# Kernel tuning notes

Measured on AMD Instinct MI355X. Metric: run time of the kernel, lower is better.

## Reference

```python
import jax, jax.numpy as jnp
import numpy as np

# dims: B batch, C tokens-per-patch, S num_patches, T input_channel(=output_channel), D d_model, P pool_size
B, C, S, T, D, P = 8, 512, 64, 128, 256, 8
EPS = 1e-5


def _cos_attn(pooled, keys):
    # pooled: (B,S,F), keys: (P,F) -> softmax over pool of cosine similarities: (B,S,P)
    pn = pooled / (jnp.linalg.norm(pooled, axis=-1, keepdims=True) + 1e-8)
    kn = keys / (jnp.linalg.norm(keys, axis=-1, keepdims=True) + 1e-8)
    return jax.nn.softmax(jnp.einsum('bsf,pf->bsp', pn, kn), axis=-1)


def setup_inputs() -> dict:
    key = jax.random.key(0)
    ks = jax.random.split(key, 5)
    sc = lambda k, shape, fan: jax.random.normal(k, shape, jnp.float32) * np.float32(1.0 / np.sqrt(fan))
    return {
        'x': jax.random.normal(ks[0], (B, C, S, T), jnp.float32),
        'gamma': jnp.ones((T,), jnp.float32),
        'beta': jnp.zeros((T,), jnp.float32),
        'keys1': sc(ks[1], (P, T), T),      # routing keys, WeightPool1
        'Wp1': sc(ks[2], (P, D, T), T),     # weight bank, T -> D
        'bp1': jnp.zeros((P, D), jnp.float32),
        'keys2': sc(ks[3], (P, D), D),      # routing keys, WeightPool2
        'Wp2': sc(ks[4], (P, T, D), D),     # weight bank, D -> T
        'bp2': jnp.zeros((P, T), jnp.float32),
    }


def reference(x, gamma, beta, keys1, Wp1, bp1, keys2, Wp2, bp2):
    # x_proj = Identity(x) since input_channel == output_channel
    # BatchNorm2d over channel T (x permuted to (B,T,S,C)) == normalize x over dims (0,1,2)
    mean = x.mean(axis=(0, 1, 2))
    var = x.var(axis=(0, 1, 2))  # biased, as torch BN training stats
    y = (x - mean) * jax.lax.rsqrt(var + EPS) * gamma + beta  # (B,C,S,T)

    # WeightPool1: pool over C, cosine-route into weight bank
    a1 = _cos_attn(y.mean(axis=1), keys1)            # (B,S,P)
    w1 = jnp.einsum('bsp,pdt->bsdt', a1, Wp1)        # (B,S,D,T)
    b1 = jnp.einsum('bsp,pd->bsd', a1, bp1)          # (B,S,D)

    y = jnp.einsum('bcst,bsdt->bcsd', y, w1) + b1[:, None]  # (B,C,S,D)
    y = jax.nn.relu(y)
    # dropout: inference mode (identity)

    # WeightPool2
    a2 = _cos_attn(y.mean(axis=1), keys2)            # (B,S,P)
    w2 = jnp.einsum('bsp,ptd->bstd', a2, Wp2)        # (B,S,T,D)
    b2 = jnp.einsum('bsp,pt->bst', a2, bp2)          # (B,S,T)

    y = jnp.einsum('bcsd,bstd->bcst', y, w2) + b2[:, None]  # (B,C,S,T)
    return (x + y, w1, w2)
```

## Files before the change

kernel.cpp:

```cpp
#include <hip/hip_runtime.h>
#include <hip/hip_bf16.h>

#define BB 8
#define CC 512
#define SS 64
#define TT 128
#define DD 256
#define PP 8
#define BS (BB*SS)
#define NSTAT (BB*CC*SS)
#define EPSV 1e-5f

typedef float f32x4 __attribute__((ext_vector_type(4)));
typedef __bf16 bf16x8 __attribute__((ext_vector_type(8)));

__device__ __forceinline__ unsigned short f2bf(float f) {
  unsigned u = __float_as_uint(f);
  u += 0x7FFFu + ((u >> 16) & 1u);
  return (unsigned short)(u >> 16);
}
__device__ __forceinline__ float bf2f(unsigned short h) {
  return __uint_as_float(((unsigned)h) << 16);
}

__global__ __launch_bounds__(256) void k1_stats(const float* __restrict__ x,
    float* __restrict__ csum_part, float* __restrict__ ssq_part,
    unsigned short* __restrict__ xbf) {
  int bid = blockIdx.x;
  int bs = bid >> 2, cq = bid & 3;
  int b = bs >> 6, s = bs & 63;
  const float* xb = x + ((size_t)b * CC * SS + s) * TT;
  unsigned short* xo = xbf + ((size_t)b * CC * SS + s) * TT;
  int tid = threadIdx.x;
  int t4 = tid & 31, coff = tid >> 5;
  float cs0=0,cs1=0,cs2=0,cs3=0, ss0=0,ss1=0,ss2=0,ss3=0;
  #pragma unroll 8
  for (int k = 0; k < 16; k++) {
    int c = cq*128 + coff + k*8;
    float4 v = *reinterpret_cast<const float4*>(xb + (size_t)c*(SS*TT) + t4*4);
    ushort4 o; o.x=f2bf(v.x); o.y=f2bf(v.y); o.z=f2bf(v.z); o.w=f2bf(v.w);
    *reinterpret_cast<ushort4*>(xo + (size_t)c*(SS*TT) + t4*4) = o;
    cs0 += v.x; cs1 += v.y; cs2 += v.z; cs3 += v.w;
    ss0 += v.x*v.x; ss1 += v.y*v.y; ss2 += v.z*v.z; ss3 += v.w*v.w;
  }
  __shared__ float4 redC[256];
  __shared__ float4 redS[256];
  redC[tid] = make_float4(cs0,cs1,cs2,cs3);
  redS[tid] = make_float4(ss0,ss1,ss2,ss3);
  __syncthreads();
  if (tid < 32) {
    #pragma unroll
    for (int j = 1; j < 8; j++) {
      float4 a = redC[tid + j*32], bq = redS[tid + j*32];
      cs0+=a.x; cs1+=a.y; cs2+=a.z; cs3+=a.w;
      ss0+=bq.x; ss1+=bq.y; ss2+=bq.z; ss3+=bq.w;
    }
    int t0 = tid*4;
    csum_part[(size_t)(t0+0)*2048 + bid] = cs0;
    csum_part[(size_t)(t0+1)*2048 + bid] = cs1;
    csum_part[(size_t)(t0+2)*2048 + bid] = cs2;
    csum_part[(size_t)(t0+3)*2048 + bid] = cs3;
    ssq_part[(size_t)(t0+0)*2048 + bid] = ss0;
    ssq_part[(size_t)(t0+1)*2048 + bid] = ss1;
    ssq_part[(size_t)(t0+2)*2048 + bid] = ss2;
    ssq_part[(size_t)(t0+3)*2048 + bid] = ss3;
  }
}

__global__ __launch_bounds__(256) void k1b_reduce(
    const float* __restrict__ csum_part, const float* __restrict__ ssq_part,
    float* __restrict__ sumt, float* __restrict__ sumsq) {
  int t = blockIdx.x, tid = threadIdx.x;
  const float* cp = csum_part + (size_t)t*2048;
  const float* sp = ssq_part + (size_t)t*2048;
  float cs = 0.f, ss = 0.f;
  #pragma unroll
  for (int k=0;k<8;k++) { cs += cp[tid + k*256]; ss += sp[tid + k*256]; }
  #pragma unroll
  for (int off=32; off; off>>=1) { cs += __shfl_xor(cs,off); ss += __shfl_xor(ss,off); }
  __shared__ float redc[4], reds[4];
  int wave = tid >> 6, lane = tid & 63;
  if (lane == 0) { redc[wave] = cs; reds[wave] = ss; }
  __syncthreads();
  if (tid == 0) {
    sumt[t]  = redc[0]+redc[1]+redc[2]+redc[3];
    sumsq[t] = reds[0]+reds[1]+reds[2]+reds[3];
  }
}

__global__ __launch_bounds__(256) void k2_route1(
    const float* __restrict__ sumt, const float* __restrict__ sumsq,
    const float* __restrict__ csum_part, const float* __restrict__ gamma,
    const float* __restrict__ beta, const float* __restrict__ keys1,
    const float* __restrict__ Wp1, const float* __restrict__ bp1,
    float* __restrict__ w1out, unsigned short* __restrict__ w1bf,
    float* __restrict__ b1) {
  int bid = blockIdx.x;
  int bs = bid >> 2, q = bid & 3;
  int tid = threadIdx.x;
  __shared__ float a1s[PP];
  if (tid < 64) {
    float pv0, pv1;
    {
      int t = tid;
      float4 c4v = *reinterpret_cast<const float4*>(csum_part + (size_t)t*2048 + bs*4);
      float cs = c4v.x + c4v.y + c4v.z + c4v.w;
      float m = sumt[t] * (1.f/NSTAT);
      float var = sumsq[t]*(1.f/NSTAT) - m*m;
      float g = gamma[t] * rsqrtf(var + EPSV);
      pv0 = (cs*(1.f/CC) - m)*g + beta[t];
    }
    {
      int t = tid + 64;
      float4 c4v = *reinterpret_cast<const float4*>(csum_part + (size_t)t*2048 + bs*4);
      float cs = c4v.x + c4v.y + c4v.z + c4v.w;
      float m = sumt[t] * (1.f/NSTAT);
      float var = sumsq[t]*(1.f/NSTAT) - m*m;
      float g = gamma[t] * rsqrtf(var + EPSV);
      pv1 = (cs*(1.f/CC) - m)*g + beta[t];
    }
    float ssq = pv0*pv0 + pv1*pv1;
    #pragma unroll
    for (int off=32; off; off>>=1) ssq += __shfl_xor(ssq, off);
    float pn = sqrtf(ssq) + 1e-8f;
    float lg[PP];
    #pragma unroll
    for (int p=0;p<PP;p++) {
      float k0 = keys1[p*TT + tid], k1 = keys1[p*TT + tid + 64];
      float dot = pv0*k0 + pv1*k1;
      float kn = k0*k0 + k1*k1;
      #pragma unroll
      for (int off=32; off; off>>=1) { dot += __shfl_xor(dot,off); kn += __shfl_xor(kn,off); }
      lg[p] = dot / (pn * (sqrtf(kn) + 1e-8f));
    }
    if (tid == 0) {
      float mx = lg[0];
      #pragma unroll
      for (int p=1;p<PP;p++) mx = fmaxf(mx, lg[p]);
      float se = 0.f, e[PP];
      #pragma unroll
      for (int p=0;p<PP;p++){ e[p] = __expf(lg[p]-mx); se += e[p]; }
      float inv = 1.f/se;
      #pragma unroll
      for (int p=0;p<PP;p++) a1s[p] = e[p]*inv;
    }
  }
  __syncthreads();
  float a[PP];
  #pragma unroll
  for (int p=0;p<PP;p++) a[p]=a1s[p];
  #pragma unroll
  for (int i=0;i<8;i++) {
    int idx = tid + i*256;
    int dr = idx >> 5, c4 = idx & 31;
    size_t roff = (size_t)(q*64+dr)*TT + c4*4;
    size_t off = (size_t)bs*(DD*TT) + roff;
    float4 accv = make_float4(0.f,0.f,0.f,0.f);
    #pragma unroll
    for (int p=0;p<PP;p++) {
      float4 v = *reinterpret_cast<const float4*>(Wp1 + (size_t)p*(DD*TT) + roff);
      accv.x += a[p]*v.x; accv.y += a[p]*v.y; accv.z += a[p]*v.z; accv.w += a[p]*v.w;
    }
    *reinterpret_cast<float4*>(w1out + off) = accv;
    ushort4 o; o.x=f2bf(accv.x); o.y=f2bf(accv.y); o.z=f2bf(accv.z); o.w=f2bf(accv.w);
    *reinterpret_cast<ushort4*>(w1bf + off) = o;
  }
  if (tid < 64) {
    int d = q*64 + tid;
    float bacc = 0.f;
    #pragma unroll
    for (int p=0;p<PP;p++) bacc += a[p]*bp1[p*DD + d];
    b1[(size_t)bs*DD + d] = bacc;
  }
}

__global__ __launch_bounds__(512) void k3_gemm1(
    const unsigned short* __restrict__ xbf, const float* __restrict__ sumt,
    const float* __restrict__ sumsq, const float* __restrict__ gamma,
    const float* __restrict__ beta, const unsigned short* __restrict__ w1bf,
    const float* __restrict__ b1, unsigned short* __restrict__ zbf,
    float* __restrict__ p2part) {
  int bid = blockIdx.x;
  int bs = bid >> 2, mt = bid & 3;
  int b = bs >> 6, s = bs & 63;
  __shared__ unsigned short lA[128*128];
  __shared__ unsigned short lB[256*128];
  __shared__ float mean_s[TT], g_s[TT], beta_s[TT];
  int tid = threadIdx.x;
  if (tid < TT) {
    float m = sumt[tid]*(1.f/NSTAT);
    float var = sumsq[tid]*(1.f/NSTAT) - m*m;
    mean_s[tid] = m;
    g_s[tid] = gamma[tid]*rsqrtf(var+EPSV);
    beta_s[tid] = beta[tid];
  }
  __syncthreads();
  char* lAc = reinterpret_cast<char*>(lA);
  char* lBc = reinterpret_cast<char*>(lB);
  auto bn2 = [&](unsigned pair, int t0) -> unsigned {
    float lo = bf2f((unsigned short)(pair & 0xFFFFu));
    float hi = bf2f((unsigned short)(pair >> 16));
    lo = (lo - mean_s[t0])*g_s[t0] + beta_s[t0];
    hi = (hi - mean_s[t0+1])*g_s[t0+1] + beta_s[t0+1];
    return ((unsigned)f2bf(hi) << 16) | (unsigned)f2bf(lo);
  };
  const unsigned short* xb = xbf + (((size_t)b*CC + mt*128)*SS + s)*TT;
  #pragma unroll
  for (int i=0;i<4;i++) {
    int flat = tid + i*512;
    int r = flat >> 4, c8 = flat & 15;
    int t0 = c8*8;
    uint4 v = *reinterpret_cast<const uint4*>(xb + (size_t)r*(SS*TT) + t0);
    uint4 o;
    o.x = bn2(v.x, t0); o.y = bn2(v.y, t0+2); o.z = bn2(v.z, t0+4); o.w = bn2(v.w, t0+6);
    unsigned addr = (unsigned)(r*256) + (((unsigned)(c8*16)) ^ (((unsigned)(r&7))<<4));
    *reinterpret_cast<uint4*>(lAc + addr) = o;
  }
  const unsigned short* wsrc = w1bf + (size_t)bs*(DD*TT);
  #pragma unroll
  for (int i=0;i<8;i++) {
    int flat = tid + i*512;
    int n = flat >> 4, ch = flat & 15;
    uint4 v = *reinterpret_cast<const uint4*>(wsrc + (size_t)flat*8);
    unsigned addr = (unsigned)(n*256) + (((unsigned)(ch*16)) ^ (((unsigned)(n&7))<<4));
    *reinterpret_cast<uint4*>(lBc + addr) = v;
  }
  __syncthreads();
  int wave = tid >> 6, lane = tid & 63;
  int wm = wave >> 2, wn = wave & 3;
  int lr = lane & 15, kg = lane >> 4;
  f32x4 zero = {0.f,0.f,0.f,0.f};
  f32x4 acc[4][4];
  #pragma unroll
  for (int m=0;m<4;m++)
    #pragma unroll
    for (int n=0;n<4;n++) acc[m][n] = zero;
  #pragma unroll
  for (int k0=0;k0<128;k0+=32) {
    bf16x8 af[4], bfr[4];
    #pragma unroll
    for (int m=0;m<4;m++) {
      int row = wm*64 + m*16 + lr;
      unsigned addr = (unsigned)(row*256) + (((unsigned)(k0*2 + kg*16)) ^ (((unsigned)(row&7))<<4));
      af[m] = *reinterpret_cast<const bf16x8*>(lAc + addr);
    }
    #pragma unroll
    for (int n=0;n<4;n++) {
      int row = wn*64 + n*16 + lr;
      unsigned addr = (unsigned)(row*256) + (((unsigned)(k0*2 + kg*16)) ^ (((unsigned)(row&7))<<4));
      bfr[n] = *reinterpret_cast<const bf16x8*>(lBc + addr);
    }
    #pragma unroll
    for (int m=0;m<4;m++)
      #pragma unroll
      for (int n=0;n<4;n++)
        acc[m][n] = __builtin_amdgcn_mfma_f32_16x16x32_bf16(af[m], bfr[n], acc[m][n], 0, 0, 0);
  }
  const float* b1p = b1 + (size_t)bs*DD;
  float* p2p = p2part + (((size_t)bid*2) + wm)*DD;
  __syncthreads();
  #pragma unroll
  for (int n=0;n<4;n++) {
    int d = wn*64 + n*16 + lr;
    float bv = b1p[d];
    float csum = 0.f;
    #pragma unroll
    for (int m=0;m<4;m++) {
      int rbase = wm*64 + m*16 + kg*4;
      #pragma unroll
      for (int j=0;j<4;j++) {
        float v = fmaxf(acc[m][n][j] + bv, 0.f);
        lB[(rbase+j)*DD + d] = f2bf(v);
        csum += v;
      }
    }
    csum += __shfl_xor(csum, 16);
    csum += __shfl_xor(csum, 32);
    if (kg == 0) p2p[d] = csum;
  }
  __syncthreads();
  unsigned short* zb = zbf + (((size_t)b*CC + mt*128)*SS + s)*DD;
  #pragma unroll
  for (int i=0;i<8;i++) {
    int flat = tid + i*512;
    int r = flat >> 5, ch = flat & 31;
    uint4 v = *reinterpret_cast<const uint4*>(lBc + flat*16);
    *reinterpret_cast<uint4*>(zb + (size_t)r*(SS*DD) + ch*8) = v;
  }
}

__global__ __launch_bounds__(256) void k4_route2(
    const float* __restrict__ p2part, const float* __restrict__ keys2,
    const float* __restrict__ Wp2, const float* __restrict__ bp2,
    float* __restrict__ w2out, unsigned short* __restrict__ w2bf,
    float* __restrict__ b2) {
  int bid = blockIdx.x;
  int bs = bid >> 2, q = bid & 3;
  int tid = threadIdx.x;
  __shared__ float a2s[PP];
  if (tid < 64) {
    float pv[4]; float ssq = 0.f;
    #pragma unroll
    for (int j=0;j<4;j++) {
      int d = tid + 64*j;
      float s8 = 0.f;
      #pragma unroll
      for (int r=0;r<8;r++) s8 += p2part[((size_t)bs*8 + r)*DD + d];
      pv[j] = s8 * (1.f/CC);
      ssq += pv[j]*pv[j];
    }
    #pragma unroll
    for (int off=32; off; off>>=1) ssq += __shfl_xor(ssq, off);
    float pn = sqrtf(ssq) + 1e-8f;
    float lg[PP];
    #pragma unroll
    for (int p=0;p<PP;p++) {
      float dot = 0.f, kn = 0.f;
      #pragma unroll
      for (int j=0;j<4;j++) {
        int d = tid + 64*j;
        float kv = keys2[p*DD + d];
        dot += pv[j]*kv; kn += kv*kv;
      }
      #pragma unroll
      for (int off=32; off; off>>=1) { dot += __shfl_xor(dot,off); kn += __shfl_xor(kn,off); }
      lg[p] = dot / (pn * (sqrtf(kn)+1e-8f));
    }
    if (tid == 0) {
      float mx = lg[0];
      #pragma unroll
      for (int p=1;p<PP;p++) mx = fmaxf(mx,lg[p]);
      float se=0.f, e[PP];
      #pragma unroll
      for (int p=0;p<PP;p++){ e[p]=__expf(lg[p]-mx); se+=e[p]; }
      float inv = 1.f/se;
      #pragma unroll
      for (int p=0;p<PP;p++) a2s[p]=e[p]*inv;
    }
  }
  __syncthreads();
  float a[PP];
  #pragma unroll
  for (int p=0;p<PP;p++) a[p]=a2s[p];
  #pragma unroll
  for (int i=0;i<8;i++) {
    int idx = tid + i*256;
    int tr = idx >> 6, c4 = idx & 63;
    size_t roff = (size_t)(q*32+tr)*DD + c4*4;
    size_t off = (size_t)bs*(TT*DD) + roff;
    float4 accv = make_float4(0.f,0.f,0.f,0.f);
    #pragma unroll
    for (int p=0;p<PP;p++) {
      float4 v = *reinterpret_cast<const float4*>(Wp2 + (size_t)p*(TT*DD) + roff);
      accv.x += a[p]*v.x; accv.y += a[p]*v.y; accv.z += a[p]*v.z; accv.w += a[p]*v.w;
    }
    *reinterpret_cast<float4*>(w2out + off) = accv;
    ushort4 o; o.x=f2bf(accv.x); o.y=f2bf(accv.y); o.z=f2bf(accv.z); o.w=f2bf(accv.w);
    *reinterpret_cast<ushort4*>(w2bf + off) = o;
  }
  if (tid < 32) {
    int t = q*32 + tid;
    float bacc = 0.f;
    #pragma unroll
    for (int p=0;p<PP;p++) bacc += a[p]*bp2[p*TT + t];
    b2[(size_t)bs*TT + t] = bacc;
  }
}

__global__ __launch_bounds__(512) void k5_gemm2(
    const unsigned short* __restrict__ zbf, const unsigned short* __restrict__ w2bf,
    const float* __restrict__ b2, const unsigned short* __restrict__ xbf,
    float* __restrict__ out) {
  int bid = blockIdx.x;
  int bs = bid >> 2, mt = bid & 3;
  int b = bs >> 6, s = bs & 63;
  __shared__ unsigned short lA[128*256];
  __shared__ unsigned short lB[128*256];
  int tid = threadIdx.x;
  char* lAc = reinterpret_cast<char*>(lA);
  char* lBc = reinterpret_cast<char*>(lB);
  const unsigned short* za = zbf + (((size_t)b*CC + mt*128)*SS + s)*DD;
  #pragma unroll
  for (int i=0;i<8;i++) {
    int flat = tid + i*512;
    int r = flat >> 5, ch = flat & 31;
    uint4 v = *reinterpret_cast<const uint4*>(za + (size_t)r*(SS*DD) + ch*8);
    unsigned addr = (unsigned)(r*512) + (((unsigned)(ch*16)) ^ (((unsigned)(r&7))<<4));
    *reinterpret_cast<uint4*>(lAc + addr) = v;
  }
  const unsigned short* wsrc = w2bf + (size_t)bs*(TT*DD);
  #pragma unroll
  for (int i=0;i<8;i++) {
    int flat = tid + i*512;
    int r = flat >> 5, ch = flat & 31;
    uint4 v = *reinterpret_cast<const uint4*>(wsrc + (size_t)flat*8);
    unsigned addr = (unsigned)(r*512) + (((unsigned)(ch*16)) ^ (((unsigned)(r&7))<<4));
    *reinterpret_cast<uint4*>(lBc + addr) = v;
  }
  __syncthreads();
  int wave = tid >> 6, lane = tid & 63;
  int wm = wave >> 2, wn = wave & 3;
  int lr = lane & 15, kg = lane >> 4;
  f32x4 zero = {0.f,0.f,0.f,0.f};
  f32x4 acc[4][2];
  #pragma unroll
  for (int m=0;m<4;m++)
    #pragma unroll
    for (int n=0;n<2;n++) acc[m][n] = zero;
  #pragma unroll
  for (int k0=0;k0<256;k0+=32) {
    bf16x8 af[4], bfr[2];
    #pragma unroll
    for (int m=0;m<4;m++) {
      int row = wm*64 + m*16 + lr;
      unsigned addr = (unsigned)(row*512) + (((unsigned)(k0*2 + kg*16)) ^ (((unsigned)(row&7))<<4));
      af[m] = *reinterpret_cast<const bf16x8*>(lAc + addr);
    }
    #pragma unroll
    for (int n=0;n<2;n++) {
      int row = wn*32 + n*16 + lr;
      unsigned addr = (unsigned)(row*512) + (((unsigned)(k0*2 + kg*16)) ^ (((unsigned)(row&7))<<4));
      bfr[n] = *reinterpret_cast<const bf16x8*>(lBc + addr);
    }
    #pragma unroll
    for (int m=0;m<4;m++)
      #pragma unroll
      for (int n=0;n<2;n++)
        acc[m][n] = __builtin_amdgcn_mfma_f32_16x16x32_bf16(af[m], bfr[n], acc[m][n], 0, 0, 0);
  }
  const float* b2p = b2 + (size_t)bs*TT;
  const unsigned short* xb = xbf + (((size_t)b*CC + mt*128)*SS + s)*TT;
  float* ob = out + (((size_t)b*CC + mt*128)*SS + s)*TT;
  #pragma unroll
  for (int n=0;n<2;n++) {
    int t = wn*32 + n*16 + lr;
    float bv = b2p[t];
    #pragma unroll
    for (int m=0;m<4;m++) {
      int rbase = wm*64 + m*16 + kg*4;
      #pragma unroll
      for (int j=0;j<4;j++) {
        size_t off = (size_t)(rbase+j)*(SS*TT) + t;
        ob[off] = acc[m][n][j] + bv + bf2f(xb[off]);
      }
    }
  }
}

extern "C" void kernel_launch(void* const* d_in, const int* in_sizes, int n_in,
                              void* d_out, int out_size, void* d_ws, size_t ws_size,
                              hipStream_t stream) {
  (void)in_sizes; (void)n_in; (void)out_size; (void)ws_size;
  const float* x     = (const float*)d_in[0];
  const float* gamma = (const float*)d_in[1];
  const float* beta  = (const float*)d_in[2];
  const float* keys1 = (const float*)d_in[3];
  const float* Wp1   = (const float*)d_in[4];
  const float* bp1   = (const float*)d_in[5];
  const float* keys2 = (const float*)d_in[6];
  const float* Wp2   = (const float*)d_in[7];
  const float* bp2   = (const float*)d_in[8];
  float* out = (float*)d_out;
  char* ws = (char*)d_ws;

  float* sumt        = (float*)(ws + 0);
  float* sumsq       = (float*)(ws + 512);
  float* csum_part   = (float*)(ws + 1024);
  float* ssq_part    = (float*)(ws + 1049600);
  float* p2part      = (float*)(ws + 2098176);
  float* b1          = (float*)(ws + 6292480);
  float* b2          = (float*)(ws + 6816768);
  unsigned short* w1bf = (unsigned short*)(ws + 7078912);
  unsigned short* w2bf = (unsigned short*)(ws + 40633344);
  unsigned short* xbf  = (unsigned short*)(ws + 74187776);
  unsigned short* zbf  = (unsigned short*)(ws + 141296640);

  float* w1out = out + 33554432;
  float* w2out = out + 50331648;

  k1_stats  <<<BS*4, 256, 0, stream>>>(x, csum_part, ssq_part, xbf);
  k1b_reduce<<<TT,   256, 0, stream>>>(csum_part, ssq_part, sumt, sumsq);
  k2_route1 <<<BS*4, 256, 0, stream>>>(sumt, sumsq, csum_part, gamma, beta, keys1, Wp1, bp1,
                                       w1out, w1bf, b1);
  k3_gemm1  <<<BS*4, 512, 0, stream>>>(xbf, sumt, sumsq, gamma, beta, w1bf, b1, zbf, p2part);
  k4_route2 <<<BS*4, 256, 0, stream>>>(p2part, keys2, Wp2, bp2, w2out, w2bf, b2);
  k5_gemm2  <<<BS*4, 512, 0, stream>>>(zbf, w2bf, b2, xbf, out);
}
```

Measured before the change: 291.0 us.

## Split routing from weight mixing, widen GEMM blocks, stage epilogues through LDS

Routing kernels now only compute the attention coefficients and biases. A new mixing kernel loads each Wp chunk once into registers and reuses it across 32 (b,s) pairs, instead of rereading the pool for every pair. The stats partials are transposed so writes are coalesced float4 stores. Both GEMM kernels move to 1024 threads with global loads issued before the LDS stores. k5 stages its output through swizzled LDS so the residual add and stores are vectorized and coalesced. This adds two kernel launches and raises register and LDS pressure per block.

New measurement: 348.0 us. +19.6%, slower.

```diff
diff --git a/kernel.cpp b/kernel.cpp
--- a/kernel.cpp
+++ b/kernel.cpp
@@ -55,15 +55,8 @@
       cs0+=a.x; cs1+=a.y; cs2+=a.z; cs3+=a.w;
       ss0+=bq.x; ss1+=bq.y; ss2+=bq.z; ss3+=bq.w;
     }
-    int t0 = tid*4;
-    csum_part[(size_t)(t0+0)*2048 + bid] = cs0;
-    csum_part[(size_t)(t0+1)*2048 + bid] = cs1;
-    csum_part[(size_t)(t0+2)*2048 + bid] = cs2;
-    csum_part[(size_t)(t0+3)*2048 + bid] = cs3;
-    ssq_part[(size_t)(t0+0)*2048 + bid] = ss0;
-    ssq_part[(size_t)(t0+1)*2048 + bid] = ss1;
-    ssq_part[(size_t)(t0+2)*2048 + bid] = ss2;
-    ssq_part[(size_t)(t0+3)*2048 + bid] = ss3;
+    *reinterpret_cast<float4*>(csum_part + (size_t)bid*TT + tid*4) = make_float4(cs0,cs1,cs2,cs3);
+    *reinterpret_cast<float4*>(ssq_part  + (size_t)bid*TT + tid*4) = make_float4(ss0,ss1,ss2,ss3);
   }
 }
 
@@ -71,11 +64,13 @@
     const float* __restrict__ csum_part, const float* __restrict__ ssq_part,
     float* __restrict__ sumt, float* __restrict__ sumsq) {
   int t = blockIdx.x, tid = threadIdx.x;
-  const float* cp = csum_part + (size_t)t*2048;
-  const float* sp = ssq_part + (size_t)t*2048;
   float cs = 0.f, ss = 0.f;
   #pragma unroll
-  for (int k=0;k<8;k++) { cs += cp[tid + k*256]; ss += sp[tid + k*256]; }
+  for (int k=0;k<8;k++) {
+    int bidk = tid + k*256;
+    cs += csum_part[(size_t)bidk*TT + t];
+    ss += ssq_part[(size_t)bidk*TT + t];
+  }
   #pragma unroll
   for (int off=32; off; off>>=1) { cs += __shfl_xor(cs,off); ss += __shfl_xor(ss,off); }
   __shared__ float redc[4], reds[4];
@@ -88,23 +83,20 @@
   }
 }
 
-__global__ __launch_bounds__(256) void k2_route1(
+__global__ __launch_bounds__(256) void k2a_route1(
     const float* __restrict__ sumt, const float* __restrict__ sumsq,
     const float* __restrict__ csum_part, const float* __restrict__ gamma,
     const float* __restrict__ beta, const float* __restrict__ keys1,
-    const float* __restrict__ Wp1, const float* __restrict__ bp1,
-    float* __restrict__ w1out, unsigned short* __restrict__ w1bf,
+    const float* __restrict__ bp1, float* __restrict__ a1g,
     float* __restrict__ b1) {
-  int bid = blockIdx.x;
-  int bs = bid >> 2, q = bid & 3;
-  int tid = threadIdx.x;
+  int bs = blockIdx.x, tid = threadIdx.x;
   __shared__ float a1s[PP];
   if (tid < 64) {
     float pv0, pv1;
     {
       int t = tid;
-      float4 c4v = *reinterpret_cast<const float4*>(csum_part + (size_t)t*2048 + bs*4);
-      float cs = c4v.x + c4v.y + c4v.z + c4v.w;
+      float cs = csum_part[(size_t)(bs*4+0)*TT+t] + csum_part[(size_t)(bs*4+1)*TT+t]
+               + csum_part[(size_t)(bs*4+2)*TT+t] + csum_part[(size_t)(bs*4+3)*TT+t];
       float m = sumt[t] * (1.f/NSTAT);
       float var = sumsq[t]*(1.f/NSTAT) - m*m;
       float g = gamma[t] * rsqrtf(var + EPSV);
@@ -112,8 +104,8 @@
     }
     {
       int t = tid + 64;
-      float4 c4v = *reinterpret_cast<const float4*>(csum_part + (size_t)t*2048 + bs*4);
-      float cs = c4v.x + c4v.y + c4v.z + c4v.w;
+      float cs = csum_part[(size_t)(bs*4+0)*TT+t] + csum_part[(size_t)(bs*4+1)*TT+t]
+               + csum_part[(size_t)(bs*4+2)*TT+t] + csum_part[(size_t)(bs*4+3)*TT+t];
       float m = sumt[t] * (1.f/NSTAT);
       float var = sumsq[t]*(1.f/NSTAT) - m*m;
       float g = gamma[t] * rsqrtf(var + EPSV);
@@ -146,35 +138,44 @@
     }
   }
   __syncthreads();
-  float a[PP];
-  #pragma unroll
-  for (int p=0;p<PP;p++) a[p]=a1s[p];
-  #pragma unroll
-  for (int i=0;i<8;i++) {
-    int idx = tid + i*256;
-    int dr = idx >> 5, c4 = idx & 31;
-    size_t roff = (size_t)(q*64+dr)*TT + c4*4;
-    size_t off = (size_t)bs*(DD*TT) + roff;
-    float4 accv = make_float4(0.f,0.f,0.f,0.f);
+  if (tid < PP) a1g[bs*PP + tid] = a1s[tid];
+  float bacc = 0.f;
+  #pragma unroll
+  for (int p=0;p<PP;p++) bacc += a1s[p]*bp1[p*DD + tid];
+  b1[(size_t)bs*DD + tid] = bacc;
+}
+
+__global__ __launch_bounds__(256) void kmix(
+    const float* __restrict__ Wp, const float* __restrict__ ag,
+    float* __restrict__ wout, unsigned short* __restrict__ wbf) {
+  int bid = blockIdx.x;
+  int chunk = bid & 31;
+  int bsg = bid >> 5;
+  int tid = threadIdx.x;
+  int e = chunk*1024 + tid*4;
+  float4 w[PP];
+  #pragma unroll
+  for (int p=0;p<PP;p++) w[p] = *reinterpret_cast<const float4*>(Wp + (size_t)p*32768 + e);
+  __shared__ float as[256];
+  as[tid] = ag[bsg*256 + tid];
+  __syncthreads();
+  #pragma unroll 4
+  for (int i=0;i<32;i++) {
+    int bs = bsg*32 + i;
+    float4 acc = make_float4(0.f,0.f,0.f,0.f);
     #pragma unroll
     for (int p=0;p<PP;p++) {
-      float4 v = *reinterpret_cast<const float4*>(Wp1 + (size_t)p*(DD*TT) + roff);
-      accv.x += a[p]*v.x; accv.y += a[p]*v.y; accv.z += a[p]*v.z; accv.w += a[p]*v.w;
-    }
-    *reinterpret_cast<float4*>(w1out + off) = accv;
-    ushort4 o; o.x=f2bf(accv.x); o.y=f2bf(accv.y); o.z=f2bf(accv.z); o.w=f2bf(accv.w);
-    *reinterpret_cast<ushort4*>(w1bf + off) = o;
-  }
-  if (tid < 64) {
-    int d = q*64 + tid;
-    float bacc = 0.f;
-    #pragma unroll
-    for (int p=0;p<PP;p++) bacc += a[p]*bp1[p*DD + d];
-    b1[(size_t)bs*DD + d] = bacc;
-  }
-}
-
-__global__ __launch_bounds__(512) void k3_gemm1(
+      float a = as[i*8+p];
+      acc.x += a*w[p].x; acc.y += a*w[p].y; acc.z += a*w[p].z; acc.w += a*w[p].w;
+    }
+    size_t off = (size_t)bs*32768 + e;
+    *reinterpret_cast<float4*>(wout + off) = acc;
+    ushort4 o; o.x=f2bf(acc.x); o.y=f2bf(acc.y); o.z=f2bf(acc.z); o.w=f2bf(acc.w);
+    *reinterpret_cast<ushort4*>(wbf + off) = o;
+  }
+}
+
+__global__ __launch_bounds__(1024) void k3_gemm1(
     const unsigned short* __restrict__ xbf, const float* __restrict__ sumt,
     const float* __restrict__ sumsq, const float* __restrict__ gamma,
     const float* __restrict__ beta, const unsigned short* __restrict__ w1bf,
@@ -187,6 +188,22 @@
   __shared__ unsigned short lB[256*128];
   __shared__ float mean_s[TT], g_s[TT], beta_s[TT];
   int tid = threadIdx.x;
+  char* lAc = reinterpret_cast<char*>(lA);
+  char* lBc = reinterpret_cast<char*>(lB);
+  const unsigned short* xb = xbf + (((size_t)b*CC + mt*128)*SS + s)*TT;
+  const unsigned short* wsrc = w1bf + (size_t)bs*(DD*TT);
+  uint4 ta[2], tb[4];
+  #pragma unroll
+  for (int i=0;i<2;i++) {
+    int flat = tid + i*1024;
+    int r = flat >> 4, c8 = flat & 15;
+    ta[i] = *reinterpret_cast<const uint4*>(xb + (size_t)r*(SS*TT) + c8*8);
+  }
+  #pragma unroll
+  for (int i=0;i<4;i++) {
+    int flat = tid + i*1024;
+    tb[i] = *reinterpret_cast<const uint4*>(wsrc + (size_t)flat*8);
+  }
   if (tid < TT) {
     float m = sumt[tid]*(1.f/NSTAT);
     float var = sumsq[tid]*(1.f/NSTAT) - m*m;
@@ -195,8 +212,13 @@
     beta_s[tid] = beta[tid];
   }
   __syncthreads();
-  char* lAc = reinterpret_cast<char*>(lA);
-  char* lBc = reinterpret_cast<char*>(lB);
+  #pragma unroll
+  for (int i=0;i<4;i++) {
+    int flat = tid + i*1024;
+    int n = flat >> 4, ch = flat & 15;
+    unsigned addr = (unsigned)(n*256) + (((unsigned)(ch*16)) ^ (((unsigned)(n&7))<<4));
+    *reinterpret_cast<uint4*>(lBc + addr) = tb[i];
+  }
   auto bn2 = [&](unsigned pair, int t0) -> unsigned {
     float lo = bf2f((unsigned short)(pair & 0xFFFFu));
     float hi = bf2f((unsigned short)(pair >> 16));
@@ -204,40 +226,30 @@
     hi = (hi - mean_s[t0+1])*g_s[t0+1] + beta_s[t0+1];
     return ((unsigned)f2bf(hi) << 16) | (unsigned)f2bf(lo);
   };
-  const unsigned short* xb = xbf + (((size_t)b*CC + mt*128)*SS + s)*TT;
-  #pragma unroll
-  for (int i=0;i<4;i++) {
-    int flat = tid + i*512;
+  #pragma unroll
+  for (int i=0;i<2;i++) {
+    int flat = tid + i*1024;
     int r = flat >> 4, c8 = flat & 15;
     int t0 = c8*8;
-    uint4 v = *reinterpret_cast<const uint4*>(xb + (size_t)r*(SS*TT) + t0);
     uint4 o;
-    o.x = bn2(v.x, t0); o.y = bn2(v.y, t0+2); o.z = bn2(v.z, t0+4); o.w = bn2(v.w, t0+6);
+    o.x = bn2(ta[i].x, t0); o.y = bn2(ta[i].y, t0+2);
+    o.z = bn2(ta[i].z, t0+4); o.w = bn2(ta[i].w, t0+6);
     unsigned addr = (unsigned)(r*256) + (((unsigned)(c8*16)) ^ (((unsigned)(r&7))<<4));
     *reinterpret_cast<uint4*>(lAc + addr) = o;
   }
-  const unsigned short* wsrc = w1bf + (size_t)bs*(DD*TT);
-  #pragma unroll
-  for (int i=0;i<8;i++) {
-    int flat = tid + i*512;
-    int n = flat >> 4, ch = flat & 15;
-    uint4 v = *reinterpret_cast<const uint4*>(wsrc + (size_t)flat*8);
-    unsigned addr = (unsigned)(n*256) + (((unsigned)(ch*16)) ^ (((unsigned)(n&7))<<4));
-    *reinterpret_cast<uint4*>(lBc + addr) = v;
-  }
   __syncthreads();
   int wave = tid >> 6, lane = tid & 63;
-  int wm = wave >> 2, wn = wave & 3;
+  int wm = wave >> 3, wn = wave & 7;
   int lr = lane & 15, kg = lane >> 4;
   f32x4 zero = {0.f,0.f,0.f,0.f};
-  f32x4 acc[4][4];
+  f32x4 acc[4][2];
   #pragma unroll
   for (int m=0;m<4;m++)
     #pragma unroll
-    for (int n=0;n<4;n++) acc[m][n] = zero;
+    for (int n=0;n<2;n++) acc[m][n] = zero;
   #pragma unroll
   for (int k0=0;k0<128;k0+=32) {
-    bf16x8 af[4], bfr[4];
+    bf16x8 af[4], bfr[2];
     #pragma unroll
     for (int m=0;m<4;m++) {
       int row = wm*64 + m*16 + lr;
@@ -245,23 +257,23 @@
       af[m] = *reinterpret_cast<const bf16x8*>(lAc + addr);
     }
     #pragma unroll
-    for (int n=0;n<4;n++) {
-      int row = wn*64 + n*16 + lr;
+    for (int n=0;n<2;n++) {
+      int row = wn*32 + n*16 + lr;
       unsigned addr = (unsigned)(row*256) + (((unsigned)(k0*2 + kg*16)) ^ (((unsigned)(row&7))<<4));
       bfr[n] = *reinterpret_cast<const bf16x8*>(lBc + addr);
     }
     #pragma unroll
     for (int m=0;m<4;m++)
       #pragma unroll
-      for (int n=0;n<4;n++)
+      for (int n=0;n<2;n++)
         acc[m][n] = __builtin_amdgcn_mfma_f32_16x16x32_bf16(af[m], bfr[n], acc[m][n], 0, 0, 0);
   }
   const float* b1p = b1 + (size_t)bs*DD;
   float* p2p = p2part + (((size_t)bid*2) + wm)*DD;
   __syncthreads();
   #pragma unroll
-  for (int n=0;n<4;n++) {
-    int d = wn*64 + n*16 + lr;
+  for (int n=0;n<2;n++) {
+    int d = wn*32 + n*16 + lr;
     float bv = b1p[d];
     float csum = 0.f;
     #pragma unroll
@@ -270,7 +282,9 @@
       #pragma unroll
       for (int j=0;j<4;j++) {
         float v = fmaxf(acc[m][n][j] + bv, 0.f);
-        lB[(rbase+j)*DD + d] = f2bf(v);
+        int row = rbase + j;
+        unsigned addr = (unsigned)(row*512) + (((unsigned)(d*2)) ^ (((unsigned)(row&7))<<4));
+        *reinterpret_cast<unsigned short*>(lBc + addr) = f2bf(v);
         csum += v;
       }
     }
@@ -281,34 +295,33 @@
   __syncthreads();
   unsigned short* zb = zbf + (((size_t)b*CC + mt*128)*SS + s)*DD;
   #pragma unroll
-  for (int i=0;i<8;i++) {
-    int flat = tid + i*512;
+  for (int i=0;i<4;i++) {
+    int flat = tid + i*1024;
     int r = flat >> 5, ch = flat & 31;
-    uint4 v = *reinterpret_cast<const uint4*>(lBc + flat*16);
+    unsigned addr = (unsigned)(r*512) + (((unsigned)(ch*16)) ^ (((unsigned)(r&7))<<4));
+    uint4 v = *reinterpret_cast<const uint4*>(lBc + addr);
     *reinterpret_cast<uint4*>(zb + (size_t)r*(SS*DD) + ch*8) = v;
   }
 }
 
-__global__ __launch_bounds__(256) void k4_route2(
+__global__ __launch_bounds__(256) void k4a_route2(
     const float* __restrict__ p2part, const float* __restrict__ keys2,
-    const float* __restrict__ Wp2, const float* __restrict__ bp2,
-    float* __restrict__ w2out, unsigned short* __restrict__ w2bf,
+    const float* __restrict__ bp2, float* __restrict__ a2g,
     float* __restrict__ b2) {
-  int bid = blockIdx.x;
-  int bs = bid >> 2, q = bid & 3;
-  int tid = threadIdx.x;
+  int bs = blockIdx.x, tid = threadIdx.x;
+  __shared__ float pvs[DD];
   __shared__ float a2s[PP];
+  {
+    float s8 = 0.f;
+    #pragma unroll
+    for (int r=0;r<8;r++) s8 += p2part[((size_t)bs*8 + r)*DD + tid];
+    pvs[tid] = s8 * (1.f/CC);
+  }
+  __syncthreads();
   if (tid < 64) {
     float pv[4]; float ssq = 0.f;
     #pragma unroll
-    for (int j=0;j<4;j++) {
-      int d = tid + 64*j;
-      float s8 = 0.f;
-      #pragma unroll
-      for (int r=0;r<8;r++) s8 += p2part[((size_t)bs*8 + r)*DD + d];
-      pv[j] = s8 * (1.f/CC);
-      ssq += pv[j]*pv[j];
-    }
+    for (int j=0;j<4;j++) { pv[j] = pvs[tid + 64*j]; ssq += pv[j]*pv[j]; }
     #pragma unroll
     for (int off=32; off; off>>=1) ssq += __shfl_xor(ssq, off);
     float pn = sqrtf(ssq) + 1e-8f;
@@ -318,8 +331,7 @@
       float dot = 0.f, kn = 0.f;
       #pragma unroll
       for (int j=0;j<4;j++) {
-        int d = tid + 64*j;
-        float kv = keys2[p*DD + d];
+        float kv = keys2[p*DD + tid + 64*j];
         dot += pv[j]*kv; kn += kv*kv;
       }
       #pragma unroll
@@ -339,35 +351,16 @@
     }
   }
   __syncthreads();
-  float a[PP];
-  #pragma unroll
-  for (int p=0;p<PP;p++) a[p]=a2s[p];
-  #pragma unroll
-  for (int i=0;i<8;i++) {
-    int idx = tid + i*256;
-    int tr = idx >> 6, c4 = idx & 63;
-    size_t roff = (size_t)(q*32+tr)*DD + c4*4;
-    size_t off = (size_t)bs*(TT*DD) + roff;
-    float4 accv = make_float4(0.f,0.f,0.f,0.f);
-    #pragma unroll
-    for (int p=0;p<PP;p++) {
-      float4 v = *reinterpret_cast<const float4*>(Wp2 + (size_t)p*(TT*DD) + roff);
-      accv.x += a[p]*v.x; accv.y += a[p]*v.y; accv.z += a[p]*v.z; accv.w += a[p]*v.w;
-    }
-    *reinterpret_cast<float4*>(w2out + off) = accv;
-    ushort4 o; o.x=f2bf(accv.x); o.y=f2bf(accv.y); o.z=f2bf(accv.z); o.w=f2bf(accv.w);
-    *reinterpret_cast<ushort4*>(w2bf + off) = o;
-  }
-  if (tid < 32) {
-    int t = q*32 + tid;
+  if (tid < PP) a2g[bs*PP + tid] = a2s[tid];
+  if (tid < TT) {
     float bacc = 0.f;
     #pragma unroll
-    for (int p=0;p<PP;p++) bacc += a[p]*bp2[p*TT + t];
-    b2[(size_t)bs*TT + t] = bacc;
-  }
-}
-
-__global__ __launch_bounds__(512) void k5_gemm2(
+    for (int p=0;p<PP;p++) bacc += a2s[p]*bp2[p*TT + tid];
+    b2[(size_t)bs*TT + tid] = bacc;
+  }
+}
+
+__global__ __launch_bounds__(1024) void k5_gemm2(
     const unsigned short* __restrict__ zbf, const unsigned short* __restrict__ w2bf,
     const float* __restrict__ b2, const unsigned short* __restrict__ xbf,
     float* __restrict__ out) {
@@ -380,39 +373,49 @@
   char* lAc = reinterpret_cast<char*>(lA);
   char* lBc = reinterpret_cast<char*>(lB);
   const unsigned short* za = zbf + (((size_t)b*CC + mt*128)*SS + s)*DD;
-  #pragma unroll
-  for (int i=0;i<8;i++) {
-    int flat = tid + i*512;
+  const unsigned short* wsrc = w2bf + (size_t)bs*(TT*DD);
+  uint4 ta[4], tb[4];
+  #pragma unroll
+  for (int i=0;i<4;i++) {
+    int flat = tid + i*1024;
     int r = flat >> 5, ch = flat & 31;
-    uint4 v = *reinterpret_cast<const uint4*>(za + (size_t)r*(SS*DD) + ch*8);
+    ta[i] = *reinterpret_cast<const uint4*>(za + (size_t)r*(SS*DD) + ch*8);
+  }
+  #pragma unroll
+  for (int i=0;i<4;i++) {
+    int flat = tid + i*1024;
+    tb[i] = *reinterpret_cast<const uint4*>(wsrc + (size_t)flat*8);
+  }
+  #pragma unroll
+  for (int i=0;i<4;i++) {
+    int flat = tid + i*1024;
+    int r = flat >> 5, ch = flat & 31;
     unsigned addr = (unsigned)(r*512) + (((unsigned)(ch*16)) ^ (((unsigned)(r&7))<<4));
-    *reinterpret_cast<uint4*>(lAc + addr) = v;
-  }
-  const unsigned short* wsrc = w2bf + (size_t)bs*(TT*DD);
-  #pragma unroll
-  for (int i=0;i<8;i++) {
-    int flat = tid + i*512;
+    *reinterpret_cast<uint4*>(lAc + addr) = ta[i];
+  }
+  #pragma unroll
+  for (int i=0;i<4;i++) {
+    int flat = tid + i*1024;
     int r = flat >> 5, ch = flat & 31;
-    uint4 v = *reinterpret_cast<const uint4*>(wsrc + (size_t)flat*8);
     unsigned addr = (unsigned)(r*512) + (((unsigned)(ch*16)) ^ (((unsigned)(r&7))<<4));
-    *reinterpret_cast<uint4*>(lBc + addr) = v;
+    *reinterpret_cast<uint4*>(lBc + addr) = tb[i];
   }
   __syncthreads();
   int wave = tid >> 6, lane = tid & 63;
   int wm = wave >> 2, wn = wave & 3;
   int lr = lane & 15, kg = lane >> 4;
   f32x4 zero = {0.f,0.f,0.f,0.f};
-  f32x4 acc[4][2];
-  #pragma unroll
-  for (int m=0;m<4;m++)
+  f32x4 acc[2][2];
+  #pragma unroll
+  for (int m=0;m<2;m++)
     #pragma unroll
     for (int n=0;n<2;n++) acc[m][n] = zero;
   #pragma unroll
   for (int k0=0;k0<256;k0+=32) {
-    bf16x8 af[4], bfr[2];
-    #pragma unroll
-    for (int m=0;m<4;m++) {
-      int row = wm*64 + m*16 + lr;
+    bf16x8 af[2], bfr[2];
+    #pragma unroll
+    for (int m=0;m<2;m++) {
+      int row = wm*32 + m*16 + lr;
       unsigned addr = (unsigned)(row*512) + (((unsigned)(k0*2 + kg*16)) ^ (((unsigned)(row&7))<<4));
       af[m] = *reinterpret_cast<const bf16x8*>(lAc + addr);
     }
@@ -423,27 +426,40 @@
       bfr[n] = *reinterpret_cast<const bf16x8*>(lBc + addr);
     }
     #pragma unroll
-    for (int m=0;m<4;m++)
+    for (int m=0;m<2;m++)
       #pragma unroll
       for (int n=0;n<2;n++)
         acc[m][n] = __builtin_amdgcn_mfma_f32_16x16x32_bf16(af[m], bfr[n], acc[m][n], 0, 0, 0);
   }
   const float* b2p = b2 + (size_t)bs*TT;
-  const unsigned short* xb = xbf + (((size_t)b*CC + mt*128)*SS + s)*TT;
-  float* ob = out + (((size_t)b*CC + mt*128)*SS + s)*TT;
+  __syncthreads();
   #pragma unroll
   for (int n=0;n<2;n++) {
     int t = wn*32 + n*16 + lr;
     float bv = b2p[t];
     #pragma unroll
-    for (int m=0;m<4;m++) {
-      int rbase = wm*64 + m*16 + kg*4;
+    for (int m=0;m<2;m++) {
+      int rbase = wm*32 + m*16 + kg*4;
       #pragma unroll
       for (int j=0;j<4;j++) {
-        size_t off = (size_t)(rbase+j)*(SS*TT) + t;
-        ob[off] = acc[m][n][j] + bv + bf2f(xb[off]);
+        int row = rbase + j;
+        unsigned addr = (unsigned)(row*512) + (((unsigned)(t*4)) ^ (((unsigned)(row&7))<<4));
+        *reinterpret_cast<float*>(lAc + addr) = acc[m][n][j] + bv;
       }
     }
+  }
+  __syncthreads();
+  const unsigned short* xb = xbf + (((size_t)b*CC + mt*128)*SS + s)*TT;
+  float* ob = out + (((size_t)b*CC + mt*128)*SS + s)*TT;
+  #pragma unroll
+  for (int i=0;i<4;i++) {
+    int flat = tid + i*1024;
+    int r = flat >> 5, c4 = flat & 31;
+    unsigned addr = (unsigned)(r*512) + (((unsigned)(c4*16)) ^ (((unsigned)(r&7))<<4));
+    float4 v = *reinterpret_cast<const float4*>(lAc + addr);
+    ushort4 xv = *reinterpret_cast<const ushort4*>(xb + (size_t)r*(SS*TT) + c4*4);
+    v.x += bf2f(xv.x); v.y += bf2f(xv.y); v.z += bf2f(xv.z); v.w += bf2f(xv.w);
+    *reinterpret_cast<float4*>(ob + (size_t)r*(SS*TT) + c4*4) = v;
   }
 }
 
@@ -468,21 +484,25 @@
   float* csum_part   = (float*)(ws + 1024);
   float* ssq_part    = (float*)(ws + 1049600);
   float* p2part      = (float*)(ws + 2098176);
-  float* b1          = (float*)(ws + 6292480);
-  float* b2          = (float*)(ws + 6816768);
-  unsigned short* w1bf = (unsigned short*)(ws + 7078912);
-  unsigned short* w2bf = (unsigned short*)(ws + 40633344);
-  unsigned short* xbf  = (unsigned short*)(ws + 74187776);
-  unsigned short* zbf  = (unsigned short*)(ws + 141296640);
+  float* a1g         = (float*)(ws + 6292480);
+  float* a2g         = (float*)(ws + 6308864);
+  float* b1          = (float*)(ws + 6325248);
+  float* b2          = (float*)(ws + 6849536);
+  unsigned short* w1bf = (unsigned short*)(ws + 7111680);
+  unsigned short* w2bf = (unsigned short*)(ws + 40666112);
+  unsigned short* xbf  = (unsigned short*)(ws + 74220544);
+  unsigned short* zbf  = (unsigned short*)(ws + 141329408);
 
   float* w1out = out + 33554432;
   float* w2out = out + 50331648;
 
-  k1_stats  <<<BS*4, 256, 0, stream>>>(x, csum_part, ssq_part, xbf);
-  k1b_reduce<<<TT,   256, 0, stream>>>(csum_part, ssq_part, sumt, sumsq);
-  k2_route1 <<<BS*4, 256, 0, stream>>>(sumt, sumsq, csum_part, gamma, beta, keys1, Wp1, bp1,
-                                       w1out, w1bf, b1);
-  k3_gemm1  <<<BS*4, 512, 0, stream>>>(xbf, sumt, sumsq, gamma, beta, w1bf, b1, zbf, p2part);
-  k4_route2 <<<BS*4, 256, 0, stream>>>(p2part, keys2, Wp2, bp2, w2out, w2bf, b2);
-  k5_gemm2  <<<BS*4, 512, 0, stream>>>(zbf, w2bf, b2, xbf, out);
-}
+  k1_stats  <<<BS*4, 256,  0, stream>>>(x, csum_part, ssq_part, xbf);
+  k1b_reduce<<<TT,   256,  0, stream>>>(csum_part, ssq_part, sumt, sumsq);
+  k2a_route1<<<BS,   256,  0, stream>>>(sumt, sumsq, csum_part, gamma, beta, keys1, bp1,
+                                        a1g, b1);
+  kmix      <<<512,  256,  0, stream>>>(Wp1, a1g, w1out, w1bf);
+  k3_gemm1  <<<BS*4, 1024, 0, stream>>>(xbf, sumt, sumsq, gamma, beta, w1bf, b1, zbf, p2part);
+  k4a_route2<<<BS,   256,  0, stream>>>(p2part, keys2, bp2, a2g, b2);
+  kmix      <<<512,  256,  0, stream>>>(Wp2, a2g, w2out, w2bf);
+  k5_gemm2  <<<BS*4, 1024, 0, stream>>>(zbf, w2bf, b2, xbf, out);
+}
```
